# Kernel optimization log

Measured on AMD Instinct MI355X. Metric: run time of the kernel, lower is better.

## Reference

```python
import jax, jax.numpy as jnp
import numpy as np

N_NODES = 50000
N_EDGES = 800000
D = 512
N_LAYERS = 3
LN_EPS = 1e-5


def _layer_norm(h, gamma, beta):
    mu = jnp.mean(h, axis=-1, keepdims=True)
    var = jnp.mean(jnp.square(h - mu), axis=-1, keepdims=True)
    return (h - mu) * jax.lax.rsqrt(var + LN_EPS) * gamma + beta


def setup_inputs() -> dict:
    key = jax.random.key(0)
    ks = jax.random.split(key, 5)
    x = jax.random.normal(ks[0], (N_NODES, D), dtype=jnp.float32)
    edge_index = jax.random.randint(ks[1], (2, N_EDGES), 0, N_NODES, dtype=jnp.int64)
    edge_weight = jax.random.uniform(ks[2], (N_EDGES,), dtype=jnp.float32)
    # GCNConv lin weights (xavier-ish scale), zero biases; LayerNorm affine params
    Ws = jax.random.normal(ks[3], (N_LAYERS, D, D), dtype=jnp.float32) * (1.0 / np.sqrt(D))
    bs = jnp.zeros((N_LAYERS, D), dtype=jnp.float32)
    gammas = jnp.ones((N_LAYERS, D), dtype=jnp.float32)
    betas = jnp.zeros((N_LAYERS, D), dtype=jnp.float32)
    return {"x": x, "edge_index": edge_index, "edge_weight": edge_weight,
            "Ws": Ws, "bs": bs, "gammas": gammas, "betas": betas}


def reference(x, edge_index, edge_weight, Ws, bs, gammas, betas):
    n = x.shape[0]
    row, col = edge_index[0], edge_index[1]  # source -> target (PyG convention)
    # add self loops with weight 1 (GCNConv add_self_loops=True)
    sl = jnp.arange(n, dtype=edge_index.dtype)
    row2 = jnp.concatenate([row, sl])
    col2 = jnp.concatenate([col, sl])
    ew = jnp.concatenate([edge_weight, jnp.ones((n,), dtype=edge_weight.dtype)])
    # symmetric normalization: D^{-1/2} A D^{-1/2}
    deg = jax.ops.segment_sum(ew, col2, num_segments=n)
    dinv = jnp.where(deg > 0, 1.0 / jnp.sqrt(jnp.where(deg > 0, deg, 1.0)), 0.0)
    norm = dinv[row2] * ew * dinv[col2]  # [E+N]

    for i in range(N_LAYERS):
        identity = x
        h = x @ Ws[i].T                       # [N, D] linear transform
        msg = norm[:, None] * h[row2]         # gather + scale per edge
        agg = jax.ops.segment_sum(msg, col2, num_segments=n) + bs[i]
        h = _layer_norm(agg, gammas[i], betas[i])
        if i < N_LAYERS - 1:
            h = jax.nn.relu(h)                # dropout=0 -> identity
        x = h + identity                      # residual (dims equal -> Identity proj)
    return x
```

## Files before the change

### kernel.cpp

```cpp
#include <hip/hip_runtime.h>
#include <hip/hip_bf16.h>
#include <stdint.h>

#define D 512
#define LN_EPS 1e-5f

typedef __attribute__((ext_vector_type(8))) short bf16x8;
typedef __attribute__((ext_vector_type(4))) float f32x4;

__device__ __forceinline__ unsigned short f32_to_bf16_bits(float x) {
    unsigned int u = __float_as_uint(x);
    u += 0x7fffu + ((u >> 16) & 1u);
    return (unsigned short)(u >> 16);
}
__device__ __forceinline__ float bf16lo(unsigned int u) { return __uint_as_float(u << 16); }
__device__ __forceinline__ float bf16hi(unsigned int u) { return __uint_as_float(u & 0xffff0000u); }

typedef const __attribute__((address_space(1))) unsigned int GU;
typedef __attribute__((address_space(3))) unsigned int LU;
__device__ __forceinline__ void gload_lds16(const void* g, void* l) {
    __builtin_amdgcn_global_load_lds((GU*)g, (LU*)l, 16, 0, 0);
}

__global__ void k_init(float* deg, int* cnt, int n) {
    int i = blockIdx.x * blockDim.x + threadIdx.x;
    if (i < n) { deg[i] = 1.0f; cnt[i] = 1; }
}

__global__ void k_deg_cnt(const int* __restrict__ col, const float* __restrict__ ew,
                          float* deg, int* cnt, int E) {
    int e = blockIdx.x * blockDim.x + threadIdx.x;
    if (e < E) {
        int c = col[e];
        atomicAdd(&deg[c], ew[e]);
        atomicAdd(&cnt[c], 1);
    }
}

__global__ __launch_bounds__(1024) void k_scan(const int* __restrict__ cnt,
                                               float* __restrict__ deg,
                                               int* __restrict__ rptr,
                                               int* __restrict__ cur, int n) {
    for (int i = threadIdx.x; i < n; i += 1024) deg[i] = rsqrtf(deg[i]);

    const int tid = threadIdx.x, lane = tid & 63, wv = tid >> 6;
    const int chunk = (n + 15) >> 4;
    const int wbeg = wv * chunk;
    const int wend = min(wbeg + chunk, n);

    int tot = 0;
    for (int i = wbeg + lane; i < wend; i += 64) tot += cnt[i];
#pragma unroll
    for (int off = 32; off > 0; off >>= 1) tot += __shfl_xor(tot, off);
    __shared__ int woff[17];
    if (lane == 0) woff[wv] = tot;
    __syncthreads();
    if (tid == 0) {
        int r = 0;
        for (int w = 0; w < 16; ++w) { int t = woff[w]; woff[w] = r; r += t; }
        woff[16] = r;
    }
    __syncthreads();

    int run = woff[wv];
    for (int base = wbeg; base < wend; base += 64) {
        int i = base + lane;
        int v = (i < wend) ? cnt[i] : 0;
        int inc = v;
#pragma unroll
        for (int off = 1; off < 64; off <<= 1) {
            int u = __shfl_up(inc, off);
            if (lane >= off) inc += u;
        }
        if (i < wend) {
            int excl = run + inc - v;
            rptr[i] = excl;
            cur[i] = excl;
        }
        run += __shfl(inc, 63);
    }
    if (tid == 0) rptr[n] = woff[16];
}

__global__ void k_fill(const int* __restrict__ row, const int* __restrict__ col,
                       const float* __restrict__ ew, const float* __restrict__ dinv,
                       int* cur, uint2* __restrict__ srcval, int N, int E) {
    int i = blockIdx.x * blockDim.x + threadIdx.x;
    if (i < N) {
        int slot = atomicAdd(&cur[i], 1);
        float d = dinv[i];
        uint2 sv; sv.x = (unsigned)i; sv.y = __float_as_uint(d * d);
        srcval[slot] = sv;
    } else if (i < N + E) {
        int e = i - N;
        int r = row[e], c = col[e];
        int slot = atomicAdd(&cur[c], 1);
        uint2 sv; sv.x = (unsigned)r;
        sv.y = __float_as_uint(dinv[r] * ew[e] * dinv[c]);
        srcval[slot] = sv;
    }
}

__global__ void k_cast4(const float4* __restrict__ in, ushort4* __restrict__ out,
                        long n4, long nin4) {
    long i = (long)blockIdx.x * blockDim.x + threadIdx.x;
    if (i >= n4) return;
    float4 v;
    if (i < nin4) v = in[i];
    else { v.x = 0.f; v.y = 0.f; v.z = 0.f; v.w = 0.f; }
    ushort4 o;
    o.x = f32_to_bf16_bits(v.x);
    o.y = f32_to_bf16_bits(v.y);
    o.z = f32_to_bf16_bits(v.z);
    o.w = f32_to_bf16_bits(v.w);
    out[i] = o;
}

__global__ __launch_bounds__(256) void k_gemm(
    const short* __restrict__ A,
    const short* __restrict__ W,
    short* __restrict__ H,
    int Mpad) {
    __shared__ short As[128 * 32];
    __shared__ short Bs[128 * 32];
    const int tid = threadIdx.x;
    const int wave = tid >> 6, lane = tid & 63;
    const int wm = (wave >> 1) * 64, wn = (wave & 1) * 64;
    const int tm = blockIdx.x * 128, tn = blockIdx.y * 128;
    f32x4 acc[4][4] = {};
    const int fr = lane & 15, fc = lane >> 4;

    const int r0 = tid >> 2, cb0 = (tid & 3) * 8;
    const short* Ab = A + (size_t)(tm + r0) * 512 + cb0;
    const short* Wb = W + (size_t)(tn + r0) * 512 + cb0;

    for (int k0 = 0; k0 < 512; k0 += 32) {
        gload_lds16(Ab + k0,                    &As[tid * 8]);
        gload_lds16(Ab + (size_t)64 * 512 + k0, &As[(tid + 256) * 8]);
        gload_lds16(Wb + k0,                    &Bs[tid * 8]);
        gload_lds16(Wb + (size_t)64 * 512 + k0, &Bs[(tid + 256) * 8]);
        __syncthreads();
        bf16x8 af[4], bfr[4];
#pragma unroll
        for (int m = 0; m < 4; ++m)
            af[m] = *(const bf16x8*)&As[(wm + m * 16 + fr) * 32 + fc * 8];
#pragma unroll
        for (int n = 0; n < 4; ++n)
            bfr[n] = *(const bf16x8*)&Bs[(wn + n * 16 + fr) * 32 + fc * 8];
#pragma unroll
        for (int m = 0; m < 4; ++m) {
#pragma unroll
            for (int n = 0; n < 4; ++n)
                acc[m][n] = __builtin_amdgcn_mfma_f32_16x16x32_bf16(af[m], bfr[n], acc[m][n], 0, 0, 0);
        }
        __syncthreads();
    }
    const int cbase = tn + wn + (lane & 15);
    const int rbase = tm + wm + fc * 4;
#pragma unroll
    for (int m = 0; m < 4; ++m) {
#pragma unroll
        for (int n = 0; n < 4; ++n) {
#pragma unroll
            for (int j = 0; j < 4; ++j) {
                int r = rbase + m * 16 + j;
                int c = cbase + n * 16;
                H[(size_t)r * 512 + c] = (short)f32_to_bf16_bits(acc[m][n][j]);
            }
        }
    }
}

__global__ __launch_bounds__(128) void k_agg_ln(
    const uint2* __restrict__ H2,
    const int* __restrict__ rptr,
    const uint2* __restrict__ srcval,
    const float4* __restrict__ bias,
    const float4* __restrict__ gamma,
    const float4* __restrict__ beta,
    uint2* __restrict__ xb,
    float4* __restrict__ out_f32,
    int last) {
    const int t = blockIdx.x;
    const int j = threadIdx.x;
    const int beg = rptr[t], end = rptr[t + 1];
    float a0 = 0.f, a1 = 0.f, a2 = 0.f, a3 = 0.f;
    for (int e = beg; e < end; ++e) {
        uint2 sv = srcval[e];
        float w = __uint_as_float(sv.y);
        uint2 u = H2[(size_t)sv.x * 128 + j];
        a0 = fmaf(w, bf16lo(u.x), a0);
        a1 = fmaf(w, bf16hi(u.x), a1);
        a2 = fmaf(w, bf16lo(u.y), a2);
        a3 = fmaf(w, bf16hi(u.y), a3);
    }
    float4 bv = bias[j];
    a0 += bv.x; a1 += bv.y; a2 += bv.z; a3 += bv.w;

    float s1 = a0 + a1 + a2 + a3;
    float s2 = a0 * a0 + a1 * a1 + a2 * a2 + a3 * a3;
#pragma unroll
    for (int off = 32; off > 0; off >>= 1) {
        s1 += __shfl_xor(s1, off);
        s2 += __shfl_xor(s2, off);
    }
    __shared__ float red[6];
    const int wv = j >> 6, ln = j & 63;
    if (ln == 0) { red[wv] = s1; red[2 + wv] = s2; }
    __syncthreads();
    if (j == 0) {
        float t1 = red[0] + red[1];
        float t2 = red[2] + red[3];
        float mean = t1 * (1.0f / 512.0f);
        float var = t2 * (1.0f / 512.0f) - mean * mean;
        red[4] = mean;
        red[5] = rsqrtf(var + LN_EPS);
    }
    __syncthreads();
    const float mean = red[4], rstd = red[5];

    float4 gv = gamma[j], btv = beta[j];
    float o0 = (a0 - mean) * rstd * gv.x + btv.x;
    float o1 = (a1 - mean) * rstd * gv.y + btv.y;
    float o2 = (a2 - mean) * rstd * gv.z + btv.z;
    float o3 = (a3 - mean) * rstd * gv.w + btv.w;
    if (!last) {
        o0 = fmaxf(o0, 0.f); o1 = fmaxf(o1, 0.f);
        o2 = fmaxf(o2, 0.f); o3 = fmaxf(o3, 0.f);
    }
    uint2 idu = xb[(size_t)t * 128 + j];
    o0 += bf16lo(idu.x); o1 += bf16hi(idu.x);
    o2 += bf16lo(idu.y); o3 += bf16hi(idu.y);

    if (last) {
        float4 ov; ov.x = o0; ov.y = o1; ov.z = o2; ov.w = o3;
        out_f32[(size_t)t * 128 + j] = ov;
    } else {
        uint2 pk;
        pk.x = ((unsigned int)f32_to_bf16_bits(o1) << 16) | f32_to_bf16_bits(o0);
        pk.y = ((unsigned int)f32_to_bf16_bits(o3) << 16) | f32_to_bf16_bits(o2);
        xb[(size_t)t * 128 + j] = pk;
    }
}

extern "C" void kernel_launch(void* const* d_in, const int* in_sizes, int n_in,
                              void* d_out, int out_size, void* d_ws, size_t ws_size,
                              hipStream_t stream) {
    const float* x0     = (const float*)d_in[0];
    const int*   ei     = (const int*)d_in[1];
    const float* ew     = (const float*)d_in[2];
    const float* Ws     = (const float*)d_in[3];
    const float* bs     = (const float*)d_in[4];
    const float* gammas = (const float*)d_in[5];
    const float* betas  = (const float*)d_in[6];

    const int N = in_sizes[0] / D;
    const int E = in_sizes[1] / 2;
    const int L = in_sizes[3] / (D * D);
    const int Mpad = (N + 127) & ~127;

    char* p = (char*)d_ws;
    auto carve = [&](size_t bytes) {
        char* q = p;
        p += (bytes + 255) & ~(size_t)255;
        return (void*)q;
    };
    short* xb     = (short*)carve((size_t)Mpad * D * 2);
    short* hb     = (short*)carve((size_t)Mpad * D * 2);
    short* wb     = (short*)carve((size_t)L * D * D * 2);
    float* dinv   = (float*)carve((size_t)N * 4);
    int*   cnt    = (int*)carve((size_t)N * 4);
    int*   rptr   = (int*)carve((size_t)(N + 1) * 4);
    int*   cur    = (int*)carve((size_t)N * 4);
    uint2* srcval = (uint2*)carve((size_t)(E + N) * 8);
    (void)ws_size; (void)n_in; (void)out_size;

    const int* rowI = ei;
    const int* colI = ei + E;

    const int nbN = (N + 255) / 256;
    const int nbE = (E + 255) / 256;
    const int nbF = (N + E + 255) / 256;

    k_init<<<nbN, 256, 0, stream>>>(dinv, cnt, N);
    k_deg_cnt<<<nbE, 256, 0, stream>>>(colI, ew, dinv, cnt, E);
    k_scan<<<1, 1024, 0, stream>>>(cnt, dinv, rptr, cur, N);
    k_fill<<<nbF, 256, 0, stream>>>(rowI, colI, ew, dinv, cur, srcval, N, E);

    {
        long n4 = (long)L * D * D / 4;
        k_cast4<<<(int)((n4 + 255) / 256), 256, 0, stream>>>(
            (const float4*)Ws, (ushort4*)wb, n4, n4);
    }
    {
        long n4 = (long)Mpad * D / 4, nin4 = (long)N * D / 4;
        k_cast4<<<(int)((n4 + 255) / 256), 256, 0, stream>>>(
            (const float4*)x0, (ushort4*)xb, n4, nin4);
    }

    for (int l = 0; l < L; ++l) {
        dim3 g(Mpad / 128, D / 128);
        k_gemm<<<g, 256, 0, stream>>>(xb, wb + (size_t)l * D * D, hb, Mpad);
        int last = (l == L - 1);
        k_agg_ln<<<N, 128, 0, stream>>>(
            (const uint2*)hb, rptr, srcval,
            (const float4*)(bs + (size_t)l * D),
            (const float4*)(gammas + (size_t)l * D),
            (const float4*)(betas + (size_t)l * D),
            (uint2*)xb, (float4*)d_out, last);
    }
}
```

Measured before the change: 753.3 us.

## Map one wavefront per node in aggregation with 16-byte gathers and shuffle-broadcast edges

The aggregate+LayerNorm kernel now gives each destination node to a single 64-lane wavefront, with four nodes per 256-thread block, instead of one 128-thread block per node. Each lane loads 8 bf16 values (uint4) per gathered row. Edge metadata is loaded cooperatively, 64 edges at a time, and broadcast with shuffles. Two independent accumulator sets are used so that two gathers are in flight. The LayerNorm reduction uses only wave shuffles, which removes the shared memory and the two block barriers. The cost is higher register pressure per lane, and high-degree nodes now serialize on one wave.

```diff
diff --git a/kernel.cpp b/kernel.cpp
--- a/kernel.cpp
+++ b/kernel.cpp
@@ -171,75 +171,123 @@
     }
 }
 
-__global__ __launch_bounds__(128) void k_agg_ln(
-    const uint2* __restrict__ H2,
+__global__ __launch_bounds__(256) void k_agg_ln(
+    const uint4* __restrict__ H4,
     const int* __restrict__ rptr,
     const uint2* __restrict__ srcval,
     const float4* __restrict__ bias,
     const float4* __restrict__ gamma,
     const float4* __restrict__ beta,
-    uint2* __restrict__ xb,
+    uint4* __restrict__ xb,
     float4* __restrict__ out_f32,
-    int last) {
-    const int t = blockIdx.x;
-    const int j = threadIdx.x;
+    int N, int last) {
+    const int wv = threadIdx.x >> 6, lane = threadIdx.x & 63;
+    const int t = blockIdx.x * 4 + wv;
+    if (t >= N) return;
     const int beg = rptr[t], end = rptr[t + 1];
-    float a0 = 0.f, a1 = 0.f, a2 = 0.f, a3 = 0.f;
-    for (int e = beg; e < end; ++e) {
-        uint2 sv = srcval[e];
-        float w = __uint_as_float(sv.y);
-        uint2 u = H2[(size_t)sv.x * 128 + j];
-        a0 = fmaf(w, bf16lo(u.x), a0);
-        a1 = fmaf(w, bf16hi(u.x), a1);
-        a2 = fmaf(w, bf16lo(u.y), a2);
-        a3 = fmaf(w, bf16hi(u.y), a3);
-    }
-    float4 bv = bias[j];
-    a0 += bv.x; a1 += bv.y; a2 += bv.z; a3 += bv.w;
-
-    float s1 = a0 + a1 + a2 + a3;
-    float s2 = a0 * a0 + a1 * a1 + a2 * a2 + a3 * a3;
+
+    float a[8], b[8];
+#pragma unroll
+    for (int i = 0; i < 8; ++i) { a[i] = 0.f; b[i] = 0.f; }
+
+    for (int base = beg; base < end; base += 64) {
+        int m = end - base;
+        if (m > 64) m = 64;
+        int idx = base + lane;
+        if (idx > end - 1) idx = end - 1;
+        uint2 svl = srcval[idx];
+        int e = 0;
+        for (; e + 2 <= m; e += 2) {
+            unsigned s0 = __shfl(svl.x, e);
+            unsigned s1 = __shfl(svl.x, e + 1);
+            float w0 = __uint_as_float(__shfl(svl.y, e));
+            float w1 = __uint_as_float(__shfl(svl.y, e + 1));
+            uint4 u0 = H4[(size_t)s0 * 64 + lane];
+            uint4 u1 = H4[(size_t)s1 * 64 + lane];
+            a[0] = fmaf(w0, bf16lo(u0.x), a[0]);
+            a[1] = fmaf(w0, bf16hi(u0.x), a[1]);
+            a[2] = fmaf(w0, bf16lo(u0.y), a[2]);
+            a[3] = fmaf(w0, bf16hi(u0.y), a[3]);
+            a[4] = fmaf(w0, bf16lo(u0.z), a[4]);
+            a[5] = fmaf(w0, bf16hi(u0.z), a[5]);
+            a[6] = fmaf(w0, bf16lo(u0.w), a[6]);
+            a[7] = fmaf(w0, bf16hi(u0.w), a[7]);
+            b[0] = fmaf(w1, bf16lo(u1.x), b[0]);
+            b[1] = fmaf(w1, bf16hi(u1.x), b[1]);
+            b[2] = fmaf(w1, bf16lo(u1.y), b[2]);
+            b[3] = fmaf(w1, bf16hi(u1.y), b[3]);
+            b[4] = fmaf(w1, bf16lo(u1.z), b[4]);
+            b[5] = fmaf(w1, bf16hi(u1.z), b[5]);
+            b[6] = fmaf(w1, bf16lo(u1.w), b[6]);
+            b[7] = fmaf(w1, bf16hi(u1.w), b[7]);
+        }
+        if (e < m) {
+            unsigned s0 = __shfl(svl.x, e);
+            float w0 = __uint_as_float(__shfl(svl.y, e));
+            uint4 u0 = H4[(size_t)s0 * 64 + lane];
+            a[0] = fmaf(w0, bf16lo(u0.x), a[0]);
+            a[1] = fmaf(w0, bf16hi(u0.x), a[1]);
+            a[2] = fmaf(w0, bf16lo(u0.y), a[2]);
+            a[3] = fmaf(w0, bf16hi(u0.y), a[3]);
+            a[4] = fmaf(w0, bf16lo(u0.z), a[4]);
+            a[5] = fmaf(w0, bf16hi(u0.z), a[5]);
+            a[6] = fmaf(w0, bf16lo(u0.w), a[6]);
+            a[7] = fmaf(w0, bf16hi(u0.w), a[7]);
+        }
+    }
+#pragma unroll
+    for (int i = 0; i < 8; ++i) a[i] += b[i];
+
+    float4 bv0 = bias[lane * 2], bv1 = bias[lane * 2 + 1];
+    a[0] += bv0.x; a[1] += bv0.y; a[2] += bv0.z; a[3] += bv0.w;
+    a[4] += bv1.x; a[5] += bv1.y; a[6] += bv1.z; a[7] += bv1.w;
+
+    float s1 = 0.f, s2 = 0.f;
+#pragma unroll
+    for (int i = 0; i < 8; ++i) { s1 += a[i]; s2 += a[i] * a[i]; }
 #pragma unroll
     for (int off = 32; off > 0; off >>= 1) {
         s1 += __shfl_xor(s1, off);
         s2 += __shfl_xor(s2, off);
     }
-    __shared__ float red[6];
-    const int wv = j >> 6, ln = j & 63;
-    if (ln == 0) { red[wv] = s1; red[2 + wv] = s2; }
-    __syncthreads();
-    if (j == 0) {
-        float t1 = red[0] + red[1];
-        float t2 = red[2] + red[3];
-        float mean = t1 * (1.0f / 512.0f);
-        float var = t2 * (1.0f / 512.0f) - mean * mean;
-        red[4] = mean;
-        red[5] = rsqrtf(var + LN_EPS);
-    }
-    __syncthreads();
-    const float mean = red[4], rstd = red[5];
-
-    float4 gv = gamma[j], btv = beta[j];
-    float o0 = (a0 - mean) * rstd * gv.x + btv.x;
-    float o1 = (a1 - mean) * rstd * gv.y + btv.y;
-    float o2 = (a2 - mean) * rstd * gv.z + btv.z;
-    float o3 = (a3 - mean) * rstd * gv.w + btv.w;
+    const float mean = s1 * (1.0f / 512.0f);
+    const float var = s2 * (1.0f / 512.0f) - mean * mean;
+    const float rstd = rsqrtf(var + LN_EPS);
+
+    float4 gv0 = gamma[lane * 2], gv1 = gamma[lane * 2 + 1];
+    float4 bt0 = beta[lane * 2], bt1 = beta[lane * 2 + 1];
+    float o[8];
+    o[0] = (a[0] - mean) * rstd * gv0.x + bt0.x;
+    o[1] = (a[1] - mean) * rstd * gv0.y + bt0.y;
+    o[2] = (a[2] - mean) * rstd * gv0.z + bt0.z;
+    o[3] = (a[3] - mean) * rstd * gv0.w + bt0.w;
+    o[4] = (a[4] - mean) * rstd * gv1.x + bt1.x;
+    o[5] = (a[5] - mean) * rstd * gv1.y + bt1.y;
+    o[6] = (a[6] - mean) * rstd * gv1.z + bt1.z;
+    o[7] = (a[7] - mean) * rstd * gv1.w + bt1.w;
     if (!last) {
-        o0 = fmaxf(o0, 0.f); o1 = fmaxf(o1, 0.f);
-        o2 = fmaxf(o2, 0.f); o3 = fmaxf(o3, 0.f);
-    }
-    uint2 idu = xb[(size_t)t * 128 + j];
-    o0 += bf16lo(idu.x); o1 += bf16hi(idu.x);
-    o2 += bf16lo(idu.y); o3 += bf16hi(idu.y);
+#pragma unroll
+        for (int i = 0; i < 8; ++i) o[i] = fmaxf(o[i], 0.f);
+    }
+    uint4 idu = xb[(size_t)t * 64 + lane];
+    o[0] += bf16lo(idu.x); o[1] += bf16hi(idu.x);
+    o[2] += bf16lo(idu.y); o[3] += bf16hi(idu.y);
+    o[4] += bf16lo(idu.z); o[5] += bf16hi(idu.z);
+    o[6] += bf16lo(idu.w); o[7] += bf16hi(idu.w);
 
     if (last) {
-        float4 ov; ov.x = o0; ov.y = o1; ov.z = o2; ov.w = o3;
-        out_f32[(size_t)t * 128 + j] = ov;
+        float4 f0, f1;
+        f0.x = o[0]; f0.y = o[1]; f0.z = o[2]; f0.w = o[3];
+        f1.x = o[4]; f1.y = o[5]; f1.z = o[6]; f1.w = o[7];
+        out_f32[(size_t)t * 128 + lane * 2] = f0;
+        out_f32[(size_t)t * 128 + lane * 2 + 1] = f1;
     } else {
-        uint2 pk;
-        pk.x = ((unsigned int)f32_to_bf16_bits(o1) << 16) | f32_to_bf16_bits(o0);
-        pk.y = ((unsigned int)f32_to_bf16_bits(o3) << 16) | f32_to_bf16_bits(o2);
-        xb[(size_t)t * 128 + j] = pk;
+        uint4 pk;
+        pk.x = ((unsigned)f32_to_bf16_bits(o[1]) << 16) | f32_to_bf16_bits(o[0]);
+        pk.y = ((unsigned)f32_to_bf16_bits(o[3]) << 16) | f32_to_bf16_bits(o[2]);
+        pk.z = ((unsigned)f32_to_bf16_bits(o[5]) << 16) | f32_to_bf16_bits(o[4]);
+        pk.w = ((unsigned)f32_to_bf16_bits(o[7]) << 16) | f32_to_bf16_bits(o[6]);
+        xb[(size_t)t * 64 + lane] = pk;
     }
 }
 
@@ -302,11 +350,11 @@
         dim3 g(Mpad / 128, D / 128);
         k_gemm<<<g, 256, 0, stream>>>(xb, wb + (size_t)l * D * D, hb, Mpad);
         int last = (l == L - 1);
-        k_agg_ln<<<N, 128, 0, stream>>>(
-            (const uint2*)hb, rptr, srcval,
+        k_agg_ln<<<(N + 3) / 4, 256, 0, stream>>>(
+            (const uint4*)hb, rptr, srcval,
             (const float4*)(bs + (size_t)l * D),
             (const float4*)(gammas + (size_t)l * D),
             (const float4*)(betas + (size_t)l * D),
-            (uint2*)xb, (float4*)d_out, last);
-    }
-}
+            (uint4*)xb, (float4*)d_out, N, last);
+    }
+}
```

Result: faster. 734.0 us (-2.6%).
